# Kernel tuning notes

Measured on AMD Instinct MI355X. Metric: run time of the kernel, lower is better.

Reference implementation:

```python
import jax, jax.numpy as jnp
import numpy as np

N_NODES = 50000
N_EDGES = 800000
IN_CH, HID, HEADS, OUT_CH = 16, 64, 4, 8
NEG_SLOPE = 0.2


def _add_self_loops(edge_index, num_nodes):
    loop = jnp.arange(num_nodes, dtype=edge_index.dtype)
    loops = jnp.stack([loop, loop])  # [2, N]
    return jnp.concatenate([edge_index, loops], axis=1)


def _gat_conv(x, src, dst, W, a_src, a_dst, bias, concat):
    """PyG-style GATConv: linear -> per-edge LeakyReLU attention -> segment
    softmax over incoming edges -> scatter-add aggregate."""
    N = x.shape[0]
    H, C = a_src.shape
    h = (x @ W).reshape(N, H, C)                      # [N,H,C]
    alpha_src = (h * a_src).sum(-1)                   # [N,H]
    alpha_dst = (h * a_dst).sum(-1)                   # [N,H]
    e = jax.nn.leaky_relu(alpha_src[src] + alpha_dst[dst], NEG_SLOPE)  # [E,H]
    # numerically stable segment softmax over edges grouped by dst
    e_max = jax.ops.segment_max(e, dst, num_segments=N)
    e_exp = jnp.exp(e - e_max[dst])
    denom = jax.ops.segment_sum(e_exp, dst, num_segments=N)
    alpha = e_exp / denom[dst]                        # [E,H]
    msg = h[src] * alpha[:, :, None]                  # [E,H,C]
    out = jax.ops.segment_sum(msg, dst, num_segments=N)  # [N,H,C]
    if concat:
        return out.reshape(N, H * C) + bias
    return out.mean(axis=1) + bias


def setup_inputs() -> dict:
    key = jax.random.key(0)
    ks = jax.random.split(key, 12)
    s = 0.1
    return {
        "x": jax.random.normal(ks[0], (N_NODES, IN_CH), jnp.float32),
        "edge_index": jax.random.randint(ks[1], (2, N_EDGES), 0, N_NODES, jnp.int64),
        "W1": jax.random.normal(ks[2], (IN_CH, HEADS * HID), jnp.float32) * s,
        "as1": jax.random.normal(ks[3], (HEADS, HID), jnp.float32) * s,
        "ad1": jax.random.normal(ks[4], (HEADS, HID), jnp.float32) * s,
        "b1": jnp.zeros((HEADS * HID,), jnp.float32),
        "W2": jax.random.normal(ks[5], (HEADS * HID, HEADS * HID), jnp.float32) * s,
        "as2": jax.random.normal(ks[6], (HEADS, HID), jnp.float32) * s,
        "ad2": jax.random.normal(ks[7], (HEADS, HID), jnp.float32) * s,
        "b2": jnp.zeros((HID,), jnp.float32),
        "Wc": jax.random.normal(ks[8], (HID, OUT_CH), jnp.float32) * s,
        "bc": jnp.zeros((OUT_CH,), jnp.float32),
    }


def reference(x, edge_index, W1, as1, ad1, b1, W2, as2, ad2, b2, Wc, bc):
    ei = _add_self_loops(edge_index, x.shape[0])
    src, dst = ei[0], ei[1]
    h = _gat_conv(x, src, dst, W1, as1, ad1, b1, concat=True)
    h = jax.nn.elu(h)
    h = _gat_conv(h, src, dst, W2, as2, ad2, b2, concat=False)
    h = jax.nn.elu(h)
    return h @ Wc + bc  # [N, OUT_CH]
```

## Files before the change

### kernel.cpp

```cpp
#include <hip/hip_runtime.h>
#include <math.h>

#define NODES   50000
#define HEADS   4
#define HID     64
#define FDIM    256
#define IN_CH   16
#define NEG_SLOPE 0.2f

typedef unsigned short ushort_t;
typedef unsigned int uint_t;
typedef __attribute__((ext_vector_type(8))) short bf16x8;
typedef __attribute__((ext_vector_type(4))) float f32x4;
typedef __attribute__((ext_vector_type(2))) float f32x2;

__device__ inline ushort_t f2bf(float f) {
    uint_t u = __float_as_uint(f);
    u += 0x7fffu + ((u >> 16) & 1u);
    return (ushort_t)(u >> 16);
}
__device__ inline void unpack2(uint_t u, float& a, float& b) {
    a = __uint_as_float(u << 16);
    b = __uint_as_float(u & 0xffff0000u);
}
__device__ inline uint_t f2h(float f) {
    _Float16 h = (_Float16)f;
    return (uint_t)*(ushort_t*)&h;
}
__device__ inline float h2f(uint_t u) {
    ushort_t us = (ushort_t)u;
    _Float16 h = *(_Float16*)&us;
    return (float)h;
}


__global__ void k_hist(const int* __restrict__ ei, int E, int N, int* __restrict__ deg) {
    int e = blockIdx.x * blockDim.x + threadIdx.x;
    int Etot = E + N;
    if (e >= Etot) return;
    int d = (e < E) ? ei[E + e] : (e - E);
    if (d >= 0 && d < N) atomicAdd(&deg[d], 1);
}

__global__ __launch_bounds__(256) void k_scanA(const int* __restrict__ deg,
                                               int* __restrict__ bsum, int N) {
    __shared__ int sh[256];
    int t = threadIdx.x;
    int i0 = blockIdx.x * 4096 + t * 16;
    int s = 0;
#pragma unroll
    for (int j = 0; j < 16; ++j) s += (i0 + j < N) ? deg[i0 + j] : 0;
    sh[t] = s;
    __syncthreads();
    for (int off = 128; off; off >>= 1) {
        if (t < off) sh[t] += sh[t + off];
        __syncthreads();
    }
    if (t == 0) bsum[blockIdx.x] = sh[0];
}

__global__ void k_scanB(int* __restrict__ bsum, int* __restrict__ rowst, int nb, int N) {
    int t = threadIdx.x;
    int orig = (t < nb) ? bsum[t] : 0;
    int v = orig;
#pragma unroll
    for (int off = 1; off < 64; off <<= 1) {
        int u = __shfl_up(v, off);
        if (t >= off) v += u;
    }
    if (t < nb) bsum[t] = v - orig;
    if (t == 63) rowst[N] = v;
}

__global__ __launch_bounds__(256) void k_scanC(const int* __restrict__ deg,
                                               const int* __restrict__ bsum,
                                               int* __restrict__ rowst,
                                               int* __restrict__ cursor, int N) {
    __shared__ int sh[256];
    int t = threadIdx.x, b = blockIdx.x;
    int i0 = b * 4096 + t * 16;
    int v[16], s = 0;
#pragma unroll
    for (int j = 0; j < 16; ++j) { v[j] = (i0 + j < N) ? deg[i0 + j] : 0; s += v[j]; }
    sh[t] = s;
    __syncthreads();
    for (int off = 1; off < 256; off <<= 1) {
        int u = (t >= off) ? sh[t - off] : 0;
        __syncthreads();
        sh[t] += u;
        __syncthreads();
    }
    int excl = sh[t] - s + bsum[b];
#pragma unroll
    for (int j = 0; j < 16; ++j) {
        if (i0 + j < N) { rowst[i0 + j] = excl; cursor[i0 + j] = excl; }
        excl += v[j];
    }
}

__global__ void k_scatter(const int* __restrict__ ei, int E, int N,
                          int* __restrict__ cursor, int2* __restrict__ csr2) {
    int e = blockIdx.x * blockDim.x + threadIdx.x;
    int Etot = E + N;
    if (e >= Etot) return;
    int s, d;
    if (e < E) { s = ei[e]; d = ei[E + e]; } else { s = d = e - E; }
    if (d < 0 || d >= N) return;
    int pos = atomicAdd(&cursor[d], 1);
    csr2[pos] = make_int2(s, d);
}


__global__ __launch_bounds__(256) void k_prep1(const float* __restrict__ x,
                                               const float* __restrict__ W1,
                                               const float* __restrict__ as1,
                                               const float* __restrict__ ad1,
                                               const float* __restrict__ W2,
                                               ushort_t* __restrict__ h,
                                               float* __restrict__ asrc,
                                               float* __restrict__ adst,
                                               ushort_t* __restrict__ W2T, int Nn) {
    int bid = blockIdx.x, t = threadIdx.x;
    if (bid >= Nn) {
        int idx = (bid - Nn) * 256 + t;
        int n = idx >> 8, k = idx & 255;
        W2T[idx] = f2bf(W2[k * FDIM + n]);
        return;
    }
    const float4* xp = (const float4*)(x + bid * IN_CH);
    float4 x0 = xp[0], x1 = xp[1], x2 = xp[2], x3 = xp[3];
    float s = x0.x * W1[t]            + x0.y * W1[FDIM + t]
            + x0.z * W1[2 * FDIM + t] + x0.w * W1[3 * FDIM + t]
            + x1.x * W1[4 * FDIM + t] + x1.y * W1[5 * FDIM + t]
            + x1.z * W1[6 * FDIM + t] + x1.w * W1[7 * FDIM + t]
            + x2.x * W1[8 * FDIM + t] + x2.y * W1[9 * FDIM + t]
            + x2.z * W1[10 * FDIM + t]+ x2.w * W1[11 * FDIM + t]
            + x3.x * W1[12 * FDIM + t]+ x3.y * W1[13 * FDIM + t]
            + x3.z * W1[14 * FDIM + t]+ x3.w * W1[15 * FDIM + t];
    h[(long)bid * FDIM + t] = f2bf(s);
    float p1 = s * as1[t];
    float p2 = s * ad1[t];
#pragma unroll
    for (int off = 1; off < 64; off <<= 1) {
        p1 += __shfl_xor(p1, off);
        p2 += __shfl_xor(p2, off);
    }
    if ((t & 63) == 0) {
        int hh = t >> 6;
        asrc[bid * 4 + hh] = p1;
        adst[bid * 4 + hh] = p2;
    }
}


__global__ __launch_bounds__(256) void k_gemm2(const ushort_t* __restrict__ A,
                                               const ushort_t* __restrict__ BT,
                                               ushort_t* __restrict__ C, int M) {
    __shared__ short As[64 * 40];
    __shared__ short Bs[64 * 40];
    int tid = threadIdx.x;
    int row0 = blockIdx.y * 64, col0 = blockIdx.x * 64;
    int wid = tid >> 6, lane = tid & 63;
    int wm = wid >> 1, wn = wid & 1;
    int quad = lane >> 4, lm = lane & 15;
    int lr = tid >> 2, lk = (tid & 3) * 8;
    f32x4 acc[2][2] = {};
    for (int k0 = 0; k0 < FDIM; k0 += 32) {
        uint4 av = {0u, 0u, 0u, 0u};
        int ar = row0 + lr;
        if (ar < M) av = *(const uint4*)(A + (long)ar * FDIM + k0 + lk);
        *(uint4*)(&As[lr * 40 + lk]) = av;
        uint4 bv = *(const uint4*)(BT + (long)(col0 + lr) * FDIM + k0 + lk);
        *(uint4*)(&Bs[lr * 40 + lk]) = bv;
        __syncthreads();
        bf16x8 a0 = *(const bf16x8*)(&As[(wm * 32 + lm) * 40 + quad * 8]);
        bf16x8 a1 = *(const bf16x8*)(&As[(wm * 32 + 16 + lm) * 40 + quad * 8]);
        bf16x8 b0 = *(const bf16x8*)(&Bs[(wn * 32 + lm) * 40 + quad * 8]);
        bf16x8 b1 = *(const bf16x8*)(&Bs[(wn * 32 + 16 + lm) * 40 + quad * 8]);
        acc[0][0] = __builtin_amdgcn_mfma_f32_16x16x32_bf16(a0, b0, acc[0][0], 0, 0, 0);
        acc[0][1] = __builtin_amdgcn_mfma_f32_16x16x32_bf16(a0, b1, acc[0][1], 0, 0, 0);
        acc[1][0] = __builtin_amdgcn_mfma_f32_16x16x32_bf16(a1, b0, acc[1][0], 0, 0, 0);
        acc[1][1] = __builtin_amdgcn_mfma_f32_16x16x32_bf16(a1, b1, acc[1][1], 0, 0, 0);
        __syncthreads();
    }
#pragma unroll
    for (int mi = 0; mi < 2; ++mi)
#pragma unroll
        for (int ni = 0; ni < 2; ++ni)
#pragma unroll
            for (int r = 0; r < 4; ++r) {
                int row = row0 + wm * 32 + mi * 16 + quad * 4 + r;
                int col = col0 + wn * 32 + ni * 16 + lm;
                if (row < M) C[(long)row * FDIM + col] = f2bf(acc[mi][ni][r]);
            }
}


__global__ void k_alpha(const ushort_t* __restrict__ h, const float* __restrict__ a_s,
                        const float* __restrict__ a_d, float* __restrict__ asrc,
                        float* __restrict__ adst, int Nn) {
    int idx = blockIdx.x * blockDim.x + threadIdx.x;
    if (idx >= Nn * HEADS) return;
    int n = idx >> 2, hh = idx & 3;
    const uint4* hp = (const uint4*)(h + (long)n * FDIM + hh * HID);
    const float* asp = a_s + hh * HID;
    const float* adp = a_d + hh * HID;
    float s1 = 0.f, s2 = 0.f;
#pragma unroll
    for (int q = 0; q < 8; ++q) {
        uint4 u = hp[q];
        float f[8];
        unpack2(u.x, f[0], f[1]); unpack2(u.y, f[2], f[3]);
        unpack2(u.z, f[4], f[5]); unpack2(u.w, f[6], f[7]);
#pragma unroll
        for (int j = 0; j < 8; ++j) { s1 += f[j] * asp[q * 8 + j]; s2 += f[j] * adp[q * 8 + j]; }
    }
    asrc[idx] = s1;
    adst[idx] = s2;
}


__global__ void k_pw(const int2* __restrict__ csr2, const float* __restrict__ asrc,
                     const float* __restrict__ adst, uint_t* __restrict__ pwb, int Etot) {
    int e = blockIdx.x * blockDim.x + threadIdx.x;
    if (e >= Etot) return;
    int2 sd = csr2[e];
    float4 av = *(const float4*)(asrc + sd.x * 4);
    float4 dv = *(const float4*)(adst + sd.y * 4);
    float t[4] = {av.x + dv.x, av.y + dv.y, av.z + dv.z, av.w + dv.w};
    uint_t sh = (uint_t)sd.x << 16;
#pragma unroll
    for (int h = 0; h < 4; ++h) {
        float tt = (t[h] > 0.f) ? t[h] : NEG_SLOPE * t[h];
        pwb[h * Etot + e] = sh | f2h(__expf(tt));
    }
}


__device__ inline void fma8(f32x2& a0, f32x2& a1, f32x2& a2, f32x2& a3,
                            uint4 hv, float pw) {
    f32x2 p = {pw, pw};
    f32x2 u;
    u.x = __uint_as_float(hv.x << 16); u.y = __uint_as_float(hv.x & 0xffff0000u);
    a0 += p * u;
    u.x = __uint_as_float(hv.y << 16); u.y = __uint_as_float(hv.y & 0xffff0000u);
    a1 += p * u;
    u.x = __uint_as_float(hv.z << 16); u.y = __uint_as_float(hv.z & 0xffff0000u);
    a2 += p * u;
    u.x = __uint_as_float(hv.w << 16); u.y = __uint_as_float(hv.w & 0xffff0000u);
    a3 += p * u;
}

__global__ __launch_bounds__(256) void k_agg(const ushort_t* __restrict__ h,
                                             const uint_t* __restrict__ pwb,
                                             const int* __restrict__ row_start,
                                             const float* __restrict__ b1,
                                             const float* __restrict__ b2,
                                             const float* __restrict__ Wc,
                                             const float* __restrict__ bc,
                                             ushort_t* __restrict__ hout,
                                             float* __restrict__ fout,
                                             int mode, int Etot, int N) {
    __shared__ float zsh[2 * FDIM];
    __shared__ float wsh[584];
    int tid  = threadIdx.x;
    int hh   = tid >> 6;
    int lane = tid & 63;
    int half = lane >> 5;
    int l32  = lane & 31;
    int g    = l32 >> 3;
    int cg   = l32 & 7;
    int d    = blockIdx.x * 2 + half;
    bool valid = d < N;

    if (!mode) {
        for (int i = tid; i < 584; i += 256)
            wsh[i] = (i < 512) ? Wc[i] : ((i < 520) ? bc[i - 512] : b2[i - 520]);
    }

    int s0 = 0, s1 = 0;
    if (valid) { s0 = row_start[d]; s1 = row_start[d + 1]; }
    int cnt  = s1 - s0;
    int maxc = max(cnt, __shfl_xor(cnt, 32));
    const uint_t* pwp = pwb + (long)hh * Etot;
    const char* hbase = (const char*)h + (hh * HID + cg * 8) * 2;

    f32x2 a0 = {0.f, 0.f}, a1 = {0.f, 0.f}, a2 = {0.f, 0.f}, a3 = {0.f, 0.f};
    float den = 0.f;

    for (int off = 0; off < maxc; off += 16) {
        int i0 = s0 + off + g;
        uint_t u0 = (i0      < s1) ? pwp[i0]      : 0u;
        uint_t u1 = (i0 + 4  < s1) ? pwp[i0 + 4]  : 0u;
        uint_t u2 = (i0 + 8  < s1) ? pwp[i0 + 8]  : 0u;
        uint_t u3 = (i0 + 12 < s1) ? pwp[i0 + 12] : 0u;
        uint4 hv0 = *(const uint4*)(hbase + ((size_t)(u0 >> 16) << 9));
        uint4 hv1 = *(const uint4*)(hbase + ((size_t)(u1 >> 16) << 9));
        uint4 hv2 = *(const uint4*)(hbase + ((size_t)(u2 >> 16) << 9));
        uint4 hv3 = *(const uint4*)(hbase + ((size_t)(u3 >> 16) << 9));
        float pw0 = h2f(u0 & 0xffffu), pw1 = h2f(u1 & 0xffffu);
        float pw2 = h2f(u2 & 0xffffu), pw3 = h2f(u3 & 0xffffu);
        den += (pw0 + pw1) + (pw2 + pw3);
        fma8(a0, a1, a2, a3, hv0, pw0);
        fma8(a0, a1, a2, a3, hv1, pw1);
        fma8(a0, a1, a2, a3, hv2, pw2);
        fma8(a0, a1, a2, a3, hv3, pw3);
    }
#pragma unroll
    for (int off = 8; off <= 16; off <<= 1) {
        a0.x += __shfl_xor(a0.x, off); a0.y += __shfl_xor(a0.y, off);
        a1.x += __shfl_xor(a1.x, off); a1.y += __shfl_xor(a1.y, off);
        a2.x += __shfl_xor(a2.x, off); a2.y += __shfl_xor(a2.y, off);
        a3.x += __shfl_xor(a3.x, off); a3.y += __shfl_xor(a3.y, off);
        den  += __shfl_xor(den, off);
    }

    if (mode) {
        if (g == 0 && valid) {
            float inv = 1.f / den;
            float v[8] = {a0.x, a0.y, a1.x, a1.y, a2.x, a2.y, a3.x, a3.y};
            const float* bp = b1 + hh * HID + cg * 8;
#pragma unroll
            for (int j = 0; j < 8; ++j) {
                float t = v[j] * inv + bp[j];
                v[j] = (t > 0.f) ? t : __expf(t) - 1.f;
            }
            uint4 u;
            u.x = (uint_t)f2bf(v[0]) | ((uint_t)f2bf(v[1]) << 16);
            u.y = (uint_t)f2bf(v[2]) | ((uint_t)f2bf(v[3]) << 16);
            u.z = (uint_t)f2bf(v[4]) | ((uint_t)f2bf(v[5]) << 16);
            u.w = (uint_t)f2bf(v[6]) | ((uint_t)f2bf(v[7]) << 16);
            *(uint4*)(hout + (long)d * FDIM + hh * HID + cg * 8) = u;
        }
    } else {
        if (g == 0 && valid) {
            float inv = 1.f / den;
            float v[8] = {a0.x, a0.y, a1.x, a1.y, a2.x, a2.y, a3.x, a3.y};
            int zb = half * FDIM + hh * HID + cg * 8;
#pragma unroll
            for (int j = 0; j < 8; ++j) zsh[zb + j] = v[j] * inv;
        }
        __syncthreads();
        if (tid < 128) {
            int node = tid >> 6, c = tid & 63;
            int dd = blockIdx.x * 2 + node;
            if (dd < N) {
                const float* zp = zsh + node * FDIM;
                float zv = 0.25f * (zp[c] + zp[64 + c] + zp[128 + c] + zp[192 + c])
                         + wsh[520 + c];
                zv = (zv > 0.f) ? zv : __expf(zv) - 1.f;
                zsh[node * FDIM + c] = zv;
            }
        }
        __syncthreads();
        if (tid < 16) {
            int node = tid >> 3, o = tid & 7;
            int dd = blockIdx.x * 2 + node;
            if (dd < N) {
                float acc = wsh[512 + o];
                const float* zp = zsh + node * FDIM;
#pragma unroll 8
                for (int c = 0; c < 64; ++c) acc += zp[c] * wsh[c * 8 + o];
                fout[(long)dd * 8 + o] = acc;
            }
        }
    }
}


extern "C" void kernel_launch(void* const* d_in, const int* in_sizes, int n_in,
                              void* d_out, int out_size, void* d_ws, size_t ws_size,
                              hipStream_t stream) {
    const float* x   = (const float*)d_in[0];
    const int*   ei  = (const int*)d_in[1];
    const float* W1  = (const float*)d_in[2];
    const float* as1 = (const float*)d_in[3];
    const float* ad1 = (const float*)d_in[4];
    const float* b1  = (const float*)d_in[5];
    const float* W2  = (const float*)d_in[6];
    const float* as2 = (const float*)d_in[7];
    const float* ad2 = (const float*)d_in[8];
    const float* b2  = (const float*)d_in[9];
    const float* Wc  = (const float*)d_in[10];
    const float* bc  = (const float*)d_in[11];
    float* out = (float*)d_out;

    const int N = NODES;
    const int E = in_sizes[1] / 2;
    const int Etot = E + N;

    char* ws = (char*)d_ws;
    size_t off = 0;
    auto alloc = [&](size_t bytes) {
        void* p = ws + off;
        off = (off + bytes + 255) & ~(size_t)255;
        return p;
    };
    ushort_t* hbf    = (ushort_t*)alloc((size_t)N * FDIM * 2);
    ushort_t* hact   = (ushort_t*)alloc((size_t)N * FDIM * 2);
    float*    asrc   = (float*)alloc((size_t)N * HEADS * 4);
    float*    adst   = (float*)alloc((size_t)N * HEADS * 4);
    ushort_t* W2T    = (ushort_t*)alloc((size_t)FDIM * FDIM * 2);
    int*      deg    = (int*)alloc((size_t)N * 4);
    int*      rowst  = (int*)alloc((size_t)(N + 1) * 4);
    int*      cursor = (int*)alloc((size_t)N * 4);
    int*      bsum   = (int*)alloc(64 * 4);
    int2*     csr2   = (int2*)alloc((size_t)Etot * 8);
    uint_t*   pwb    = (uint_t*)alloc((size_t)Etot * HEADS * 4);

    const int tpb = 256;
    int egrid = (Etot + tpb - 1) / tpb;
    int nb = (N + 4095) / 4096;

    hipMemsetAsync(deg, 0, (size_t)N * 4, stream);
    k_hist<<<egrid, tpb, 0, stream>>>(ei, E, N, deg);
    k_scanA<<<nb, 256, 0, stream>>>(deg, bsum, N);
    k_scanB<<<1, 64, 0, stream>>>(bsum, rowst, nb, N);
    k_scanC<<<nb, 256, 0, stream>>>(deg, bsum, rowst, cursor, N);
    k_scatter<<<egrid, tpb, 0, stream>>>(ei, E, N, cursor, csr2);

    k_prep1<<<N + 256, 256, 0, stream>>>(x, W1, as1, ad1, W2, hbf, asrc, adst, W2T, N);
    k_pw<<<egrid, tpb, 0, stream>>>(csr2, asrc, adst, pwb, Etot);
    k_agg<<<(N + 1) / 2, 256, 0, stream>>>(hbf, pwb, rowst, b1, nullptr, nullptr, nullptr,
                                           hact, nullptr, 1, Etot, N);

    dim3 g2(FDIM / 64, (N + 63) / 64);
    k_gemm2<<<g2, 256, 0, stream>>>(hact, W2T, hbf, N);
    k_alpha<<<(N * HEADS + tpb - 1) / tpb, tpb, 0, stream>>>(hbf, as2, ad2, asrc, adst, N);
    k_pw<<<egrid, tpb, 0, stream>>>(csr2, asrc, adst, pwb, Etot);
    k_agg<<<(N + 1) / 2, 256, 0, stream>>>(hbf, pwb, rowst, nullptr, b2, Wc, bc,
                                           nullptr, out, 0, Etot, N);
}
```

Baseline: 403.2 us.

## Fuse edge attention weights into aggregation and merge histogram into prep kernel

Removes the separate k_pw pass that materialized per-edge, per-head packed fp16 exp weights, and instead computes LeakyReLU and exp inline inside k_agg from asrc/adst gathers. The CSR now stores only source indices (int instead of int2), and the aggregation loop processes 8 edges per thread per iteration for more memory-level parallelism. The degree histogram is folded into the prep kernel as extra blocks, which drops a launch. In exchange, the exp is recomputed once per channel group, and the asrc gathers are scattered 4-byte loads.

```diff
diff --git a/kernel.cpp b/kernel.cpp
--- a/kernel.cpp
+++ b/kernel.cpp
@@ -23,104 +23,28 @@
     a = __uint_as_float(u << 16);
     b = __uint_as_float(u & 0xffff0000u);
 }
-__device__ inline uint_t f2h(float f) {
-    _Float16 h = (_Float16)f;
-    return (uint_t)*(ushort_t*)&h;
-}
-__device__ inline float h2f(uint_t u) {
-    ushort_t us = (ushort_t)u;
-    _Float16 h = *(_Float16*)&us;
-    return (float)h;
-}
-
-
-__global__ void k_hist(const int* __restrict__ ei, int E, int N, int* __restrict__ deg) {
-    int e = blockIdx.x * blockDim.x + threadIdx.x;
-    int Etot = E + N;
-    if (e >= Etot) return;
-    int d = (e < E) ? ei[E + e] : (e - E);
-    if (d >= 0 && d < N) atomicAdd(&deg[d], 1);
-}
-
-__global__ __launch_bounds__(256) void k_scanA(const int* __restrict__ deg,
-                                               int* __restrict__ bsum, int N) {
-    __shared__ int sh[256];
-    int t = threadIdx.x;
-    int i0 = blockIdx.x * 4096 + t * 16;
-    int s = 0;
-#pragma unroll
-    for (int j = 0; j < 16; ++j) s += (i0 + j < N) ? deg[i0 + j] : 0;
-    sh[t] = s;
-    __syncthreads();
-    for (int off = 128; off; off >>= 1) {
-        if (t < off) sh[t] += sh[t + off];
-        __syncthreads();
-    }
-    if (t == 0) bsum[blockIdx.x] = sh[0];
-}
-
-__global__ void k_scanB(int* __restrict__ bsum, int* __restrict__ rowst, int nb, int N) {
-    int t = threadIdx.x;
-    int orig = (t < nb) ? bsum[t] : 0;
-    int v = orig;
-#pragma unroll
-    for (int off = 1; off < 64; off <<= 1) {
-        int u = __shfl_up(v, off);
-        if (t >= off) v += u;
-    }
-    if (t < nb) bsum[t] = v - orig;
-    if (t == 63) rowst[N] = v;
-}
-
-__global__ __launch_bounds__(256) void k_scanC(const int* __restrict__ deg,
-                                               const int* __restrict__ bsum,
-                                               int* __restrict__ rowst,
-                                               int* __restrict__ cursor, int N) {
-    __shared__ int sh[256];
-    int t = threadIdx.x, b = blockIdx.x;
-    int i0 = b * 4096 + t * 16;
-    int v[16], s = 0;
-#pragma unroll
-    for (int j = 0; j < 16; ++j) { v[j] = (i0 + j < N) ? deg[i0 + j] : 0; s += v[j]; }
-    sh[t] = s;
-    __syncthreads();
-    for (int off = 1; off < 256; off <<= 1) {
-        int u = (t >= off) ? sh[t - off] : 0;
-        __syncthreads();
-        sh[t] += u;
-        __syncthreads();
-    }
-    int excl = sh[t] - s + bsum[b];
-#pragma unroll
-    for (int j = 0; j < 16; ++j) {
-        if (i0 + j < N) { rowst[i0 + j] = excl; cursor[i0 + j] = excl; }
-        excl += v[j];
-    }
-}
-
-__global__ void k_scatter(const int* __restrict__ ei, int E, int N,
-                          int* __restrict__ cursor, int2* __restrict__ csr2) {
-    int e = blockIdx.x * blockDim.x + threadIdx.x;
-    int Etot = E + N;
-    if (e >= Etot) return;
-    int s, d;
-    if (e < E) { s = ei[e]; d = ei[E + e]; } else { s = d = e - E; }
-    if (d < 0 || d >= N) return;
-    int pos = atomicAdd(&cursor[d], 1);
-    csr2[pos] = make_int2(s, d);
-}
-
-
-__global__ __launch_bounds__(256) void k_prep1(const float* __restrict__ x,
-                                               const float* __restrict__ W1,
-                                               const float* __restrict__ as1,
-                                               const float* __restrict__ ad1,
-                                               const float* __restrict__ W2,
-                                               ushort_t* __restrict__ h,
-                                               float* __restrict__ asrc,
-                                               float* __restrict__ adst,
-                                               ushort_t* __restrict__ W2T, int Nn) {
+
+
+__global__ __launch_bounds__(256) void k_prep(const float* __restrict__ x,
+                                              const float* __restrict__ W1,
+                                              const float* __restrict__ as1,
+                                              const float* __restrict__ ad1,
+                                              const float* __restrict__ W2,
+                                              const int* __restrict__ ei, int E,
+                                              ushort_t* __restrict__ h,
+                                              float* __restrict__ asrc,
+                                              float* __restrict__ adst,
+                                              ushort_t* __restrict__ W2T,
+                                              int* __restrict__ deg, int Nn) {
     int bid = blockIdx.x, t = threadIdx.x;
+    if (bid >= Nn + 256) {
+        int e = (bid - Nn - 256) * 256 + t;
+        int Etot = E + Nn;
+        if (e >= Etot) return;
+        int d = (e < E) ? ei[E + e] : (e - E);
+        if (d >= 0 && d < Nn) atomicAdd(&deg[d], 1);
+        return;
+    }
     if (bid >= Nn) {
         int idx = (bid - Nn) * 256 + t;
         int n = idx >> 8, k = idx & 255;
@@ -150,6 +74,75 @@
         asrc[bid * 4 + hh] = p1;
         adst[bid * 4 + hh] = p2;
     }
+}
+
+
+__global__ __launch_bounds__(256) void k_scanA(const int* __restrict__ deg,
+                                               int* __restrict__ bsum, int N) {
+    __shared__ int sh[256];
+    int t = threadIdx.x;
+    int i0 = blockIdx.x * 4096 + t * 16;
+    int s = 0;
+#pragma unroll
+    for (int j = 0; j < 16; ++j) s += (i0 + j < N) ? deg[i0 + j] : 0;
+    sh[t] = s;
+    __syncthreads();
+    for (int off = 128; off; off >>= 1) {
+        if (t < off) sh[t] += sh[t + off];
+        __syncthreads();
+    }
+    if (t == 0) bsum[blockIdx.x] = sh[0];
+}
+
+__global__ void k_scanB(int* __restrict__ bsum, int* __restrict__ rowst, int nb, int N) {
+    int t = threadIdx.x;
+    int orig = (t < nb) ? bsum[t] : 0;
+    int v = orig;
+#pragma unroll
+    for (int off = 1; off < 64; off <<= 1) {
+        int u = __shfl_up(v, off);
+        if (t >= off) v += u;
+    }
+    if (t < nb) bsum[t] = v - orig;
+    if (t == 63) rowst[N] = v;
+}
+
+__global__ __launch_bounds__(256) void k_scanC(const int* __restrict__ deg,
+                                               const int* __restrict__ bsum,
+                                               int* __restrict__ rowst,
+                                               int* __restrict__ cursor, int N) {
+    __shared__ int sh[256];
+    int t = threadIdx.x, b = blockIdx.x;
+    int i0 = b * 4096 + t * 16;
+    int v[16], s = 0;
+#pragma unroll
+    for (int j = 0; j < 16; ++j) { v[j] = (i0 + j < N) ? deg[i0 + j] : 0; s += v[j]; }
+    sh[t] = s;
+    __syncthreads();
+    for (int off = 1; off < 256; off <<= 1) {
+        int u = (t >= off) ? sh[t - off] : 0;
+        __syncthreads();
+        sh[t] += u;
+        __syncthreads();
+    }
+    int excl = sh[t] - s + bsum[b];
+#pragma unroll
+    for (int j = 0; j < 16; ++j) {
+        if (i0 + j < N) { rowst[i0 + j] = excl; cursor[i0 + j] = excl; }
+        excl += v[j];
+    }
+}
+
+__global__ void k_scatter(const int* __restrict__ ei, int E, int N,
+                          int* __restrict__ cursor, int* __restrict__ csr) {
+    int e = blockIdx.x * blockDim.x + threadIdx.x;
+    int Etot = E + N;
+    if (e >= Etot) return;
+    int s, d;
+    if (e < E) { s = ei[e]; d = ei[E + e]; } else { s = d = e - E; }
+    if (d < 0 || d >= N) return;
+    int pos = atomicAdd(&cursor[d], 1);
+    csr[pos] = s;
 }
 
 
@@ -220,23 +213,6 @@
 }
 
 
-__global__ void k_pw(const int2* __restrict__ csr2, const float* __restrict__ asrc,
-                     const float* __restrict__ adst, uint_t* __restrict__ pwb, int Etot) {
-    int e = blockIdx.x * blockDim.x + threadIdx.x;
-    if (e >= Etot) return;
-    int2 sd = csr2[e];
-    float4 av = *(const float4*)(asrc + sd.x * 4);
-    float4 dv = *(const float4*)(adst + sd.y * 4);
-    float t[4] = {av.x + dv.x, av.y + dv.y, av.z + dv.z, av.w + dv.w};
-    uint_t sh = (uint_t)sd.x << 16;
-#pragma unroll
-    for (int h = 0; h < 4; ++h) {
-        float tt = (t[h] > 0.f) ? t[h] : NEG_SLOPE * t[h];
-        pwb[h * Etot + e] = sh | f2h(__expf(tt));
-    }
-}
-
-
 __device__ inline void fma8(f32x2& a0, f32x2& a1, f32x2& a2, f32x2& a3,
                             uint4 hv, float pw) {
     f32x2 p = {pw, pw};
@@ -252,15 +228,17 @@
 }
 
 __global__ __launch_bounds__(256) void k_agg(const ushort_t* __restrict__ h,
-                                             const uint_t* __restrict__ pwb,
+                                             const int* __restrict__ csr,
                                              const int* __restrict__ row_start,
+                                             const float* __restrict__ asrc,
+                                             const float* __restrict__ adst,
                                              const float* __restrict__ b1,
                                              const float* __restrict__ b2,
                                              const float* __restrict__ Wc,
                                              const float* __restrict__ bc,
                                              ushort_t* __restrict__ hout,
                                              float* __restrict__ fout,
-                                             int mode, int Etot, int N) {
+                                             int mode, int N) {
     __shared__ float zsh[2 * FDIM];
     __shared__ float wsh[584];
     int tid  = threadIdx.x;
@@ -280,31 +258,40 @@
 
     int s0 = 0, s1 = 0;
     if (valid) { s0 = row_start[d]; s1 = row_start[d + 1]; }
+    float ad = valid ? adst[d * 4 + hh] : 0.f;
+    int last = (s1 > 0) ? (s1 - 1) : 0;
     int cnt  = s1 - s0;
     int maxc = max(cnt, __shfl_xor(cnt, 32));
-    const uint_t* pwp = pwb + (long)hh * Etot;
     const char* hbase = (const char*)h + (hh * HID + cg * 8) * 2;
 
     f32x2 a0 = {0.f, 0.f}, a1 = {0.f, 0.f}, a2 = {0.f, 0.f}, a3 = {0.f, 0.f};
     float den = 0.f;
 
-    for (int off = 0; off < maxc; off += 16) {
-        int i0 = s0 + off + g;
-        uint_t u0 = (i0      < s1) ? pwp[i0]      : 0u;
-        uint_t u1 = (i0 + 4  < s1) ? pwp[i0 + 4]  : 0u;
-        uint_t u2 = (i0 + 8  < s1) ? pwp[i0 + 8]  : 0u;
-        uint_t u3 = (i0 + 12 < s1) ? pwp[i0 + 12] : 0u;
-        uint4 hv0 = *(const uint4*)(hbase + ((size_t)(u0 >> 16) << 9));
-        uint4 hv1 = *(const uint4*)(hbase + ((size_t)(u1 >> 16) << 9));
-        uint4 hv2 = *(const uint4*)(hbase + ((size_t)(u2 >> 16) << 9));
-        uint4 hv3 = *(const uint4*)(hbase + ((size_t)(u3 >> 16) << 9));
-        float pw0 = h2f(u0 & 0xffffu), pw1 = h2f(u1 & 0xffffu);
-        float pw2 = h2f(u2 & 0xffffu), pw3 = h2f(u3 & 0xffffu);
-        den += (pw0 + pw1) + (pw2 + pw3);
-        fma8(a0, a1, a2, a3, hv0, pw0);
-        fma8(a0, a1, a2, a3, hv1, pw1);
-        fma8(a0, a1, a2, a3, hv2, pw2);
-        fma8(a0, a1, a2, a3, hv3, pw3);
+    for (int off = 0; off < maxc; off += 32) {
+        int b0 = s0 + off + g;
+        int sj[8];
+#pragma unroll
+        for (int j = 0; j < 8; ++j) {
+            int i = b0 + 4 * j;
+            sj[j] = csr[(i < s1) ? i : last];
+        }
+        float tv[8];
+#pragma unroll
+        for (int j = 0; j < 8; ++j) tv[j] = asrc[sj[j] * 4 + hh];
+        uint4 hv[8];
+#pragma unroll
+        for (int j = 0; j < 8; ++j)
+            hv[j] = *(const uint4*)(hbase + ((size_t)(uint_t)sj[j] << 9));
+        float pwv[8];
+#pragma unroll
+        for (int j = 0; j < 8; ++j) {
+            float e = tv[j] + ad;
+            e = (e > 0.f) ? e : NEG_SLOPE * e;
+            pwv[j] = ((b0 + 4 * j) < s1) ? __expf(e) : 0.f;
+            den += pwv[j];
+        }
+#pragma unroll
+        for (int j = 0; j < 8; ++j) fma8(a0, a1, a2, a3, hv[j], pwv[j]);
     }
 #pragma unroll
     for (int off = 8; off <= 16; off <<= 1) {
@@ -405,29 +392,29 @@
     int*      rowst  = (int*)alloc((size_t)(N + 1) * 4);
     int*      cursor = (int*)alloc((size_t)N * 4);
     int*      bsum   = (int*)alloc(64 * 4);
-    int2*     csr2   = (int2*)alloc((size_t)Etot * 8);
-    uint_t*   pwb    = (uint_t*)alloc((size_t)Etot * HEADS * 4);
+    int*      csr    = (int*)alloc((size_t)Etot * 4);
 
     const int tpb = 256;
     int egrid = (Etot + tpb - 1) / tpb;
     int nb = (N + 4095) / 4096;
 
     hipMemsetAsync(deg, 0, (size_t)N * 4, stream);
-    k_hist<<<egrid, tpb, 0, stream>>>(ei, E, N, deg);
+
+    k_prep<<<N + 256 + egrid, tpb, 0, stream>>>(x, W1, as1, ad1, W2, ei, E,
+                                                hbf, asrc, adst, W2T, deg, N);
     k_scanA<<<nb, 256, 0, stream>>>(deg, bsum, N);
     k_scanB<<<1, 64, 0, stream>>>(bsum, rowst, nb, N);
     k_scanC<<<nb, 256, 0, stream>>>(deg, bsum, rowst, cursor, N);
-    k_scatter<<<egrid, tpb, 0, stream>>>(ei, E, N, cursor, csr2);
-
-    k_prep1<<<N + 256, 256, 0, stream>>>(x, W1, as1, ad1, W2, hbf, asrc, adst, W2T, N);
-    k_pw<<<egrid, tpb, 0, stream>>>(csr2, asrc, adst, pwb, Etot);
-    k_agg<<<(N + 1) / 2, 256, 0, stream>>>(hbf, pwb, rowst, b1, nullptr, nullptr, nullptr,
-                                           hact, nullptr, 1, Etot, N);
+    k_scatter<<<egrid, tpb, 0, stream>>>(ei, E, N, cursor, csr);
+
+    k_agg<<<(N + 1) / 2, 256, 0, stream>>>(hbf, csr, rowst, asrc, adst, b1,
+                                           nullptr, nullptr, nullptr,
+                                           hact, nullptr, 1, N);
 
     dim3 g2(FDIM / 64, (N + 63) / 64);
     k_gemm2<<<g2, 256, 0, stream>>>(hact, W2T, hbf, N);
     k_alpha<<<(N * HEADS + tpb - 1) / tpb, tpb, 0, stream>>>(hbf, as2, ad2, asrc, adst, N);
-    k_pw<<<egrid, tpb, 0, stream>>>(csr2, asrc, adst, pwb, Etot);
-    k_agg<<<(N + 1) / 2, 256, 0, stream>>>(hbf, pwb, rowst, nullptr, b2, Wc, bc,
-                                           nullptr, out, 0, Etot, N);
-}
+
+    k_agg<<<(N + 1) / 2, 256, 0, stream>>>(hbf, csr, rowst, asrc, adst, nullptr,
+                                           b2, Wc, bc, nullptr, out, 0, N);
+}
```

Result: no change. 400.3 us (-0.7%).
